# Kernel tuning notes

Measured on AMD Instinct MI355X. Metric: run time of the kernel, lower is better.

## Reference

```python
import jax, jax.numpy as jnp
import numpy as np

E, D_IN, D_OUT, RANK, ALPHA = 8, 2048, 2048, 8, 8.0
SCALING = ALPHA / RANK


def setup_inputs() -> dict:
    key = jax.random.key(0)
    ks = jax.random.split(key, 7)
    x = jax.random.normal(ks[0], (2, 4096, D_IN), dtype=jnp.float32)
    # base linear fc: weight [d_out, d_in], bias [d_out]
    Wf = jax.random.normal(ks[1], (D_OUT, D_IN), dtype=jnp.float32) / np.sqrt(D_IN)
    bf = jax.random.normal(ks[2], (D_OUT,), dtype=jnp.float32) * 0.01
    # router: weight [E, d_in], bias [E]
    Wr = jax.random.normal(ks[3], (E, D_IN), dtype=jnp.float32) / np.sqrt(D_IN)
    br = jnp.zeros((E,), dtype=jnp.float32)
    # stacked LoRA factors: A [E, rank, d_in] (kaiming-uniform-like), B [E, d_out, rank]
    # (original inits lora_B to zeros; use small random values so grads are non-trivial)
    A = jax.random.uniform(ks[4], (E, RANK, D_IN), dtype=jnp.float32,
                           minval=-1.0, maxval=1.0) / np.sqrt(D_IN)
    Bm = jax.random.normal(ks[5], (E, D_OUT, RANK), dtype=jnp.float32) * 0.02
    return {"x": x, "Wf": Wf, "bf": bf, "Wr": Wr, "br": br, "A": A, "Bm": Bm}


def reference(x, Wf, bf, Wr, br, A, Bm):
    # base output: x @ Wf^T + bf  -> [B, T, d_out]
    base = jnp.einsum('btd,od->bto', x, Wf) + bf
    # router softmax over experts -> [B, T, E]
    logits = jnp.einsum('btd,ed->bte', x, Wr) + br
    w = jax.nn.softmax(logits, axis=-1)
    # all-expert low-rank projection: h = x @ A_e^T -> [B, T, E, rank]
    h = jnp.einsum('btd,erd->bter', x, A)
    # up-project and fuse routing-weighted accumulation -> [B, T, d_out]
    lora = SCALING * jnp.einsum('bter,eor,bte->bto', h, Bm, w)
    return base + lora, w
```

## Files before the change

### kernel.cpp

```cpp
#include <hip/hip_runtime.h>
#include <hip/hip_bf16.h>

#define BT      8192
#define DIN     2048
#define DOUT    2048
#define NEXP    8
#define RANK    8
#define KX      2112
#define NSPLIT  4
#define HLD     72
#define SCALING 1.0f
#define SLOT    32768

typedef __bf16 bf16x8 __attribute__((ext_vector_type(8)));
typedef __bf16 bf16x4 __attribute__((ext_vector_type(4)));
typedef float  f32x4  __attribute__((ext_vector_type(4)));

#define XB_OFF     0
#define XB_BYTES   (BT * KX * 2)
#define WB_OFF     (XB_OFF + XB_BYTES)
#define WB_BYTES   (DOUT * KX * 2)
#define ACAT_OFF   (WB_OFF + WB_BYTES)
#define ACAT_BYTES (128 * DIN * 2)
#define HP_OFF     (ACAT_OFF + ACAT_BYTES)
#define HP_BYTES   (NSPLIT * BT * HLD * 4)

__device__ __forceinline__ void gload_lds16(const void* g, void* l) {
    __builtin_amdgcn_global_load_lds(
        (__attribute__((address_space(1))) void*)(g),
        (__attribute__((address_space(3))) void*)(l),
        16, 0, 0);
}

#define MFMA16(a, b, c) __builtin_amdgcn_mfma_f32_16x16x32_bf16((a), (b), (c), 0, 0, 0)

__global__ __launch_bounds__(256) void mole_prep(
    const float* __restrict__ Wf, const float* __restrict__ Bm,
    const float* __restrict__ Wr, const float* __restrict__ A,
    __bf16* __restrict__ WB, __bf16* __restrict__ ACAT)
{
    const int i = blockIdx.x * 256 + threadIdx.x;
    const int R1 = DOUT * (DIN / 4);
    const int R2 = DOUT * 64;
    if (i < R1) {
        const int o = i >> 9, c4 = i & 511;
        float4 v = ((const float4*)Wf)[(size_t)o * 512 + c4];
        bf16x4 b; b[0] = (__bf16)v.x; b[1] = (__bf16)v.y; b[2] = (__bf16)v.z; b[3] = (__bf16)v.w;
        *(bf16x4*)&WB[(size_t)o * KX + (c4 << 2)] = b;
    } else if (i < R1 + R2) {
        const int j = i - R1;
        const int o = j >> 6, c = j & 63;
        const int e = c >> 3, r = c & 7;
        WB[(size_t)o * KX + DIN + c] = (__bf16)Bm[((size_t)e * DOUT + o) * RANK + r];
    } else {
        const int j = i - (R1 + R2);
        const int r = j >> 9, c4 = j & 511;
        float4 v;
        if (r < 8)        v = ((const float4*)Wr)[(size_t)r * 512 + c4];
        else if (r < 72)  v = ((const float4*)A)[(size_t)(r - 8) * 512 + c4];
        else              v = make_float4(0.f, 0.f, 0.f, 0.f);
        bf16x4 b; b[0] = (__bf16)v.x; b[1] = (__bf16)v.y; b[2] = (__bf16)v.z; b[3] = (__bf16)v.w;
        *(bf16x4*)&ACAT[(size_t)r * DIN + (c4 << 2)] = b;
    }
}

__global__ __launch_bounds__(256) void mole_hconv(
    const float* __restrict__ x, const __bf16* __restrict__ ACAT,
    __bf16* __restrict__ XB, float* __restrict__ HP)
{
    __shared__ __align__(16) __bf16 Xs[128][32];
    __shared__ __align__(16) __bf16 Bs[128][32];

    const int tid = threadIdx.x;
    const int wv  = tid >> 6, ln = tid & 63;
    const int wr  = wv >> 1, wc = wv & 1;
    const size_t m0 = (size_t)blockIdx.x * 128;
    const int kStart = blockIdx.z * (DIN / NSPLIT);
    float* C = HP + (size_t)blockIdx.z * BT * HLD;

    const int xr = tid >> 3;
    const int xc = (tid & 7) << 2;
    const float* gx  = x  + (m0 + xr) * (size_t)DIN + kStart + xc;
    __bf16*      gxb = XB + (m0 + xr) * (size_t)KX  + kStart + xc;

    const int srow = (wv << 4) + (ln >> 2);
    const int scol = (ln & 3) << 3;
    const __bf16* gB0 = ACAT + srow * (size_t)DIN + kStart + scol;
    const __bf16* gB1 = gB0 + (size_t)64 * DIN;
    __bf16* lB0 = &Bs[(wv << 4)][0];
    __bf16* lB1 = &Bs[64 + (wv << 4)][0];

    f32x4 acc[4][4] = {};
    const int fr = ln & 15;
    const int fk = (ln >> 4) << 3;

    for (int ks = 0; ks < (DIN / NSPLIT) / 32; ++ks) {
        gload_lds16(gB0, lB0);
        gload_lds16(gB1, lB1);
        gB0 += 32; gB1 += 32;
        #pragma unroll
        for (int j = 0; j < 4; ++j) {
            float4 v = *(const float4*)(gx + (size_t)(32 * j) * DIN + 32 * ks);
            bf16x4 b; b[0] = (__bf16)v.x; b[1] = (__bf16)v.y;
            b[2] = (__bf16)v.z; b[3] = (__bf16)v.w;
            *(bf16x4*)&Xs[xr + 32 * j][xc] = b;
            *(bf16x4*)(gxb + (size_t)(32 * j) * KX + 32 * ks) = b;
        }
        __syncthreads();

        bf16x8 af[4], bfr[4];
        #pragma unroll
        for (int m = 0; m < 4; ++m)
            af[m] = *(const bf16x8*)&Xs[(wr << 6) + (m << 4) + fr][fk];
        #pragma unroll
        for (int n = 0; n < 4; ++n)
            bfr[n] = *(const bf16x8*)&Bs[(wc << 6) + (n << 4) + fr][fk];
        #pragma unroll
        for (int m = 0; m < 4; ++m)
            #pragma unroll
            for (int n = 0; n < 4; ++n)
                acc[m][n] = MFMA16(af[m], bfr[n], acc[m][n]);
        __syncthreads();
    }

    const int cr = (ln >> 4) << 2;
    const int cc = ln & 15;
    #pragma unroll
    for (int n = 0; n < 4; ++n) {
        const int col = (wc << 6) + (n << 4) + cc;
        if (col < HLD) {
            #pragma unroll
            for (int m = 0; m < 4; ++m) {
                const size_t row = m0 + (wr << 6) + (m << 4) + cr;
                #pragma unroll
                for (int r = 0; r < 4; ++r)
                    C[(row + r) * (size_t)HLD + col] = acc[m][n][r];
            }
        }
    }
}

__global__ __launch_bounds__(256) void mole_softmax_g(
    const float* __restrict__ HP, const float* __restrict__ br,
    float* __restrict__ wOut, __bf16* __restrict__ XB)
{
    const int t   = blockIdx.x * 4 + (threadIdx.x >> 6);
    const int tid = threadIdx.x & 63;
    float h = 0.0f;
    #pragma unroll
    for (int sp = 0; sp < NSPLIT; ++sp)
        h += HP[((size_t)sp * BT + t) * HLD + 8 + tid];

    float lg[NEXP];
    #pragma unroll
    for (int e = 0; e < NEXP; ++e) {
        lg[e] = br[e];
        #pragma unroll
        for (int sp = 0; sp < NSPLIT; ++sp)
            lg[e] += HP[((size_t)sp * BT + t) * HLD + e];
    }
    float mx = lg[0];
    #pragma unroll
    for (int e = 1; e < NEXP; ++e) mx = fmaxf(mx, lg[e]);
    float ex[NEXP], den = 0.0f;
    #pragma unroll
    for (int e = 0; e < NEXP; ++e) { ex[e] = expf(lg[e] - mx); den += ex[e]; }

    const float w_my = ex[tid >> 3] / den;
    XB[(size_t)t * KX + DIN + tid] = (__bf16)(SCALING * w_my * h);
    if (tid < NEXP) wOut[(size_t)t * NEXP + tid] = ex[tid] / den;
}

__global__ __launch_bounds__(512, 1) void mole_gemm256(
    const __bf16* __restrict__ XBp, const __bf16* __restrict__ WBp,
    float* __restrict__ C, const float* __restrict__ bias)
{
    __shared__ __align__(16) char smem[131072];

    const int tid = threadIdx.x;
    const int wv  = tid >> 6, l = tid & 63;
    const int wm  = wv >> 2, wn = wv & 3;
    const int bid = blockIdx.x;
    const int xcd = bid & 7, ib = bid >> 3;
    const int tm = xcd * 4 + (ib & 3), tn = ib >> 2;
    const size_t m0 = (size_t)tm * 256, n0 = (size_t)tn * 256;

    const int op = wv >> 2, ww = wv & 3;
    const __bf16* gstage = (op == 0 ? XBp + (m0 + ww * 64) * KX
                                    : WBp + (n0 + ww * 64) * KX)
                         + (size_t)(l >> 2) * KX + (((l & 3) ^ ((l >> 3) & 3)) << 3);
    const int stageBase = op * 16384 + ww * 4096;

    const int fr = l & 15, fq = l >> 4;
    const int swz = (fq ^ ((fr >> 1) & 3)) << 4;
    const int aByte = (wm * 128 + fr) * 64 + swz;
    const int bByte = 16384 + (wn * 64 + fr) * 64 + swz;

    f32x4 acc[8][4] = {};
    bf16x8 fa0[8], fb0[4], fa1[8], fb1[4];

#define STAGE(S)                                                              \
    {                                                                         \
        char* dst = smem + ((S) & 3) * SLOT + stageBase;                      \
        const __bf16* g = gstage + (size_t)(S) * 32;                          \
        _Pragma("unroll")                                                     \
        for (int j = 0; j < 4; ++j)                                           \
            gload_lds16(g + (size_t)j * 16 * KX, dst + j * 1024);             \
    }

#define READS(S, FA, FB)                                                      \
    {                                                                         \
        const char* slot = smem + ((S) & 3) * SLOT;                           \
        _Pragma("unroll")                                                     \
        for (int nf = 0; nf < 4; ++nf)                                        \
            FB[nf] = *(const bf16x8*)(slot + bByte + nf * 1024);              \
        _Pragma("unroll")                                                     \
        for (int mf = 0; mf < 8; ++mf)                                        \
            FA[mf] = *(const bf16x8*)(slot + aByte + mf * 1024);              \
    }

#define STEP(S, VMN, DOSTAGE, DOREAD, FAc, FBc, FAn, FBn)                     \
    {                                                                         \
        asm volatile("s_waitcnt vmcnt(" #VMN ")" ::: "memory");               \
        __builtin_amdgcn_s_barrier();                                         \
        if (DOREAD) READS((S) + 1, FAn, FBn);                                 \
        if (DOSTAGE) STAGE((S) + 3);                                          \
        __builtin_amdgcn_sched_barrier(0);                                    \
        __builtin_amdgcn_s_setprio(1);                                        \
        _Pragma("unroll")                                                     \
        for (int mf = 0; mf < 8; ++mf)                                        \
            _Pragma("unroll")                                                 \
            for (int nf = 0; nf < 4; ++nf)                                    \
                acc[mf][nf] = MFMA16(FAc[mf], FBc[nf], acc[mf][nf]);          \
        __builtin_amdgcn_s_setprio(0);                                        \
    }

    STAGE(0); STAGE(1); STAGE(2);
    asm volatile("s_waitcnt vmcnt(8)" ::: "memory");
    __builtin_amdgcn_s_barrier();
    READS(0, fa0, fb0);

    #pragma unroll 1
    for (int s = 0; s < 62; s += 2) {
        STEP(s,     4, true, true, fa0, fb0, fa1, fb1);
        STEP(s + 1, 4, true, true, fa1, fb1, fa0, fb0);
    }
    STEP(62, 4, true,  true,  fa0, fb0, fa1, fb1);
    STEP(63, 4, false, true,  fa1, fb1, fa0, fb0);
    STEP(64, 0, false, true,  fa0, fb0, fa1, fb1);
    STEP(65, 0, false, false, fa1, fb1, fa0, fb0);
#undef STEP
#undef READS
#undef STAGE

    const size_t crow = m0 + wm * 128 + fq * 4;
    const size_t ccol = n0 + wn * 64 + fr;
    #pragma unroll
    for (int nf = 0; nf < 4; ++nf) {
        const float bv = bias[ccol + nf * 16];
        #pragma unroll
        for (int mf = 0; mf < 8; ++mf) {
            float* cp = C + (crow + (size_t)mf * 16) * DOUT + ccol + nf * 16;
            #pragma unroll
            for (int i = 0; i < 4; ++i)
                cp[(size_t)i * DOUT] = acc[mf][nf][i] + bv;
        }
    }
}

extern "C" void kernel_launch(void* const* d_in, const int* in_sizes, int n_in,
                              void* d_out, int out_size, void* d_ws, size_t ws_size,
                              hipStream_t stream) {
    const float* x  = (const float*)d_in[0];
    const float* Wf = (const float*)d_in[1];
    const float* bf = (const float*)d_in[2];
    const float* Wr = (const float*)d_in[3];
    const float* br = (const float*)d_in[4];
    const float* A  = (const float*)d_in[5];
    const float* Bm = (const float*)d_in[6];

    float* out0 = (float*)d_out;
    float* wOut = out0 + (size_t)BT * DOUT;

    char* ws = (char*)d_ws;
    __bf16* XB   = (__bf16*)(ws + XB_OFF);
    __bf16* WB   = (__bf16*)(ws + WB_OFF);
    __bf16* ACAT = (__bf16*)(ws + ACAT_OFF);
    float*  HP   = (float*)(ws + HP_OFF);

    mole_prep<<<4864, 256, 0, stream>>>(Wf, Bm, Wr, A, WB, ACAT);
    mole_hconv<<<dim3(64, 1, NSPLIT), 256, 0, stream>>>(x, ACAT, XB, HP);
    mole_softmax_g<<<BT / 4, 256, 0, stream>>>(HP, br, wOut, XB);
    mole_gemm256<<<256, 512, 0, stream>>>(XB, WB, out0, bf);
}
```

Before: 103.5 us.

## Restructure GEMM main loop into K=64 double-buffered quarter-tile ping-pong schedule

Replaces the 4-slot K=32 LDS ring with two 64 KB buffers holding K=64 tiles, using a new XOR swizzle over 128-byte rows. Each K-tile's MFMA work is split into four quadrant phases interleaved with partial global-to-LDS loads for the next tile and barrier/waitcnt fences. The aim is to halve the number of iterations, cut per-K-step barrier overhead, and better overlap loads with MFMA. The cost is more barriers per tile and a hand-tuned waitcnt schedule that is fragile to get right.

```diff
diff --git a/kernel.cpp b/kernel.cpp
--- a/kernel.cpp
+++ b/kernel.cpp
@@ -10,7 +10,6 @@
 #define NSPLIT  4
 #define HLD     72
 #define SCALING 1.0f
-#define SLOT    32768
 
 typedef __bf16 bf16x8 __attribute__((ext_vector_type(8)));
 typedef __bf16 bf16x4 __attribute__((ext_vector_type(4)));
@@ -185,73 +184,136 @@
     const int tm = xcd * 4 + (ib & 3), tn = ib >> 2;
     const size_t m0 = (size_t)tm * 256, n0 = (size_t)tn * 256;
 
-    const int op = wv >> 2, ww = wv & 3;
-    const __bf16* gstage = (op == 0 ? XBp + (m0 + ww * 64) * KX
-                                    : WBp + (n0 + ww * 64) * KX)
-                         + (size_t)(l >> 2) * KX + (((l & 3) ^ ((l >> 3) & 3)) << 3);
-    const int stageBase = op * 16384 + ww * 4096;
+    const __bf16* gA = XBp + (m0 + (l >> 3)) * KX + (((l & 7) ^ (l >> 3)) << 3);
+    const __bf16* gB = WBp + (n0 + (l >> 3)) * KX + (((l & 7) ^ (l >> 3)) << 3);
+    const int wv8 = wv * 8;
+    const int rbB = ((wv & 3) * 8) + ((wv >> 2) * 64);
 
     const int fr = l & 15, fq = l >> 4;
-    const int swz = (fq ^ ((fr >> 1) & 3)) << 4;
-    const int aByte = (wm * 128 + fr) * 64 + swz;
-    const int bByte = 16384 + (wn * 64 + fr) * 64 + swz;
+    const int sw0 = ((fq)     ^ (fr & 7)) << 4;
+    const int sw1 = ((4 + fq) ^ (fr & 7)) << 4;
+    const int aOff = (wm * 128 + fr) * 128;
+    const int bOff = 32768 + (wn * 64 + fr) * 128;
 
     f32x4 acc[8][4] = {};
-    bf16x8 fa0[8], fb0[4], fa1[8], fb1[4];
-
-#define STAGE(S)                                                              \
-    {                                                                         \
-        char* dst = smem + ((S) & 3) * SLOT + stageBase;                      \
-        const __bf16* g = gstage + (size_t)(S) * 32;                          \
+    bf16x8 fa[4][2], fa2[4][2], fb[2][2], fb2[2][2];
+
+#define GLA(RB, T, BUF)                                                       \
+    gload_lds16(gA + (size_t)((RB) + wv8) * KX + (size_t)(T) * 64,            \
+                smem + (BUF) * 65536 + ((RB) + wv8) * 128)
+#define GLB(RB, T, BUF)                                                       \
+    gload_lds16(gB + (size_t)((RB) + rbB) * KX + (size_t)(T) * 64,            \
+                smem + (BUF) * 65536 + 32768 + ((RB) + rbB) * 128)
+#define ST_AQ1(T, BUF) { GLA(0, T, BUF);  GLA(128, T, BUF); }
+#define ST_AQ2(T, BUF) { GLA(64, T, BUF); GLA(192, T, BUF); }
+#define ST_BH1(T, BUF) { GLB(0, T, BUF);  GLB(128, T, BUF); }
+#define ST_BH2(T, BUF) { GLB(32, T, BUF); GLB(160, T, BUF); }
+
+#define RD_FA(ARR, B0, PB)                                                    \
+    _Pragma("unroll")                                                         \
+    for (int mf = 0; mf < 4; ++mf) {                                          \
+        const char* a_ = smem + (PB) * 65536 + aOff + ((B0) + mf) * 2048;     \
+        ARR[mf][0] = *(const bf16x8*)(a_ + sw0);                              \
+        ARR[mf][1] = *(const bf16x8*)(a_ + sw1);                              \
+    }
+#define RD_FB(ARR, B0, PB)                                                    \
+    _Pragma("unroll")                                                         \
+    for (int nf = 0; nf < 2; ++nf) {                                          \
+        const char* b_ = smem + (PB) * 65536 + bOff + ((B0) + nf) * 2048;     \
+        ARR[nf][0] = *(const bf16x8*)(b_ + sw0);                              \
+        ARR[nf][1] = *(const bf16x8*)(b_ + sw1);                              \
+    }
+#define MM(FA, FB, MB, NB)                                                    \
+    __builtin_amdgcn_s_setprio(1);                                            \
+    _Pragma("unroll")                                                         \
+    for (int kk = 0; kk < 2; ++kk)                                            \
         _Pragma("unroll")                                                     \
-        for (int j = 0; j < 4; ++j)                                           \
-            gload_lds16(g + (size_t)j * 16 * KX, dst + j * 1024);             \
-    }
-
-#define READS(S, FA, FB)                                                      \
-    {                                                                         \
-        const char* slot = smem + ((S) & 3) * SLOT;                           \
-        _Pragma("unroll")                                                     \
-        for (int nf = 0; nf < 4; ++nf)                                        \
-            FB[nf] = *(const bf16x8*)(slot + bByte + nf * 1024);              \
-        _Pragma("unroll")                                                     \
-        for (int mf = 0; mf < 8; ++mf)                                        \
-            FA[mf] = *(const bf16x8*)(slot + aByte + mf * 1024);              \
-    }
-
-#define STEP(S, VMN, DOSTAGE, DOREAD, FAc, FBc, FAn, FBn)                     \
-    {                                                                         \
-        asm volatile("s_waitcnt vmcnt(" #VMN ")" ::: "memory");               \
-        __builtin_amdgcn_s_barrier();                                         \
-        if (DOREAD) READS((S) + 1, FAn, FBn);                                 \
-        if (DOSTAGE) STAGE((S) + 3);                                          \
-        __builtin_amdgcn_sched_barrier(0);                                    \
-        __builtin_amdgcn_s_setprio(1);                                        \
-        _Pragma("unroll")                                                     \
-        for (int mf = 0; mf < 8; ++mf)                                        \
+        for (int mf = 0; mf < 4; ++mf)                                        \
             _Pragma("unroll")                                                 \
-            for (int nf = 0; nf < 4; ++nf)                                    \
-                acc[mf][nf] = MFMA16(FAc[mf], FBc[nf], acc[mf][nf]);          \
-        __builtin_amdgcn_s_setprio(0);                                        \
-    }
-
-    STAGE(0); STAGE(1); STAGE(2);
-    asm volatile("s_waitcnt vmcnt(8)" ::: "memory");
-    __builtin_amdgcn_s_barrier();
-    READS(0, fa0, fb0);
+            for (int nf = 0; nf < 2; ++nf)                                    \
+                acc[(MB) + mf][(NB) + nf] =                                   \
+                    MFMA16(FA[mf][kk], FB[nf][kk], acc[(MB) + mf][(NB) + nf]);\
+    __builtin_amdgcn_s_setprio(0);
+#define MIDBAR { __builtin_amdgcn_s_barrier();                                \
+                 asm volatile("s_waitcnt lgkmcnt(0)" ::: "memory");           \
+                 __builtin_amdgcn_sched_barrier(0); }
+#define ENDBAR __builtin_amdgcn_s_barrier();
+#define LG8    asm volatile("s_waitcnt lgkmcnt(8)" ::: "memory");
+#define VMC(N) asm volatile("s_waitcnt vmcnt(" #N ")" ::: "memory");
+
+    ST_AQ1(0, 0); ST_BH1(0, 0); ST_BH2(0, 0); ST_AQ2(0, 0);
+    ST_AQ1(1, 1); ST_BH1(1, 1); ST_BH2(1, 1);
+    VMC(6); ENDBAR;
 
     #pragma unroll 1
-    for (int s = 0; s < 62; s += 2) {
-        STEP(s,     4, true, true, fa0, fb0, fa1, fb1);
-        STEP(s + 1, 4, true, true, fa1, fb1, fa0, fb0);
-    }
-    STEP(62, 4, true,  true,  fa0, fb0, fa1, fb1);
-    STEP(63, 4, false, true,  fa1, fb1, fa0, fb0);
-    STEP(64, 0, false, true,  fa0, fb0, fa1, fb1);
-    STEP(65, 0, false, false, fa1, fb1, fa0, fb0);
-#undef STEP
-#undef READS
-#undef STAGE
+    for (int i = 0; i < 15; ++i) {
+        const int t = 2 * i;
+        RD_FA(fa, 0, 0); RD_FB(fb, 0, 0);
+        ST_AQ2(t + 1, 1);
+        LG8; MIDBAR; MM(fa, fb, 0, 0); ENDBAR;
+        RD_FB(fb2, 2, 0);
+        ST_AQ1(t + 2, 0);
+        MIDBAR; MM(fa, fb2, 0, 2); ENDBAR;
+        RD_FA(fa2, 4, 0);
+        ST_BH1(t + 2, 0);
+        MIDBAR; MM(fa2, fb, 4, 0); ENDBAR;
+        ST_BH2(t + 2, 0);
+        MIDBAR; MM(fa2, fb2, 4, 2); VMC(6); ENDBAR;
+        RD_FA(fa, 0, 1); RD_FB(fb, 0, 1);
+        ST_AQ2(t + 2, 0);
+        LG8; MIDBAR; MM(fa, fb, 0, 0); ENDBAR;
+        RD_FB(fb2, 2, 1);
+        ST_AQ1(t + 3, 1);
+        MIDBAR; MM(fa, fb2, 0, 2); ENDBAR;
+        RD_FA(fa2, 4, 1);
+        ST_BH1(t + 3, 1);
+        MIDBAR; MM(fa2, fb, 4, 0); ENDBAR;
+        ST_BH2(t + 3, 1);
+        MIDBAR; MM(fa2, fb2, 4, 2); VMC(6); ENDBAR;
+    }
+    {
+        RD_FA(fa, 0, 0); RD_FB(fb, 0, 0);
+        ST_AQ2(31, 1);
+        LG8; MIDBAR; MM(fa, fb, 0, 0); ENDBAR;
+        RD_FB(fb2, 2, 0);
+        ST_AQ1(32, 0);
+        MIDBAR; MM(fa, fb2, 0, 2); ENDBAR;
+        RD_FA(fa2, 4, 0);
+        ST_BH1(32, 0);
+        MIDBAR; MM(fa2, fb, 4, 0); ENDBAR;
+        ST_BH2(32, 0);
+        MIDBAR; MM(fa2, fb2, 4, 2); VMC(6); ENDBAR;
+        RD_FA(fa, 0, 1); RD_FB(fb, 0, 1);
+        ST_AQ2(32, 0);
+        LG8; MIDBAR; MM(fa, fb, 0, 0); ENDBAR;
+        RD_FB(fb2, 2, 1);
+        MIDBAR; MM(fa, fb2, 0, 2); ENDBAR;
+        RD_FA(fa2, 4, 1);
+        MIDBAR; MM(fa2, fb, 4, 0); ENDBAR;
+        MIDBAR; MM(fa2, fb2, 4, 2); VMC(4); ENDBAR;
+    }
+    {
+        RD_FA(fa, 0, 0); RD_FB(fb, 0, 0);
+        LG8; MIDBAR; MM(fa, fb, 0, 0); VMC(2); ENDBAR;
+        RD_FB(fb2, 2, 0);
+        MIDBAR; MM(fa, fb2, 0, 2); VMC(0); ENDBAR;
+        RD_FA(fa2, 4, 0);
+        MIDBAR; MM(fa2, fb, 4, 0); ENDBAR;
+        MM(fa2, fb2, 4, 2);
+    }
+#undef GLA
+#undef GLB
+#undef ST_AQ1
+#undef ST_AQ2
+#undef ST_BH1
+#undef ST_BH2
+#undef RD_FA
+#undef RD_FB
+#undef MM
+#undef MIDBAR
+#undef ENDBAR
+#undef LG8
+#undef VMC
 
     const size_t crow = m0 + wm * 128 + fq * 4;
     const size_t ccol = n0 + wn * 64 + fr;
```

After: 100.9 us (median of 3 runs). 1.03x faster.

## Fuse router/LoRA-A projection with softmax and gating into one kernel

Applied to the files above, without the earlier changes.

Replaces the split-K hconv kernel and the separate softmax kernel with one kernel that processes 16 tokens per block over the full K range. Router softmax and the gated LoRA intermediate are computed in shared memory and written straight into the bf16 activation buffer. This drops the fp32 partial-sum workspace round-trip and one launch, and gives 512 blocks instead of 256. The cost is that every block re-reads the whole 128x2048 ACAT matrix and issues only two MFMAs per K step per wave, so the kernel may be bound by loads and barriers.

```diff
diff --git a/kernel.cpp b/kernel.cpp
--- a/kernel.cpp
+++ b/kernel.cpp
@@ -7,8 +7,6 @@
 #define NEXP    8
 #define RANK    8
 #define KX      2112
-#define NSPLIT  4
-#define HLD     72
 #define SCALING 1.0f
 #define SLOT    32768
 
@@ -22,8 +20,6 @@
 #define WB_BYTES   (DOUT * KX * 2)
 #define ACAT_OFF   (WB_OFF + WB_BYTES)
 #define ACAT_BYTES (128 * DIN * 2)
-#define HP_OFF     (ACAT_OFF + ACAT_BYTES)
-#define HP_BYTES   (NSPLIT * BT * HLD * 4)
 
 __device__ __forceinline__ void gload_lds16(const void* g, void* l) {
     __builtin_amdgcn_global_load_lds(
@@ -64,111 +60,103 @@
     }
 }
 
-__global__ __launch_bounds__(256) void mole_hconv(
+__global__ __launch_bounds__(256) void mole_hfuse(
     const float* __restrict__ x, const __bf16* __restrict__ ACAT,
-    __bf16* __restrict__ XB, float* __restrict__ HP)
+    const float* __restrict__ br,
+    __bf16* __restrict__ XB, float* __restrict__ wOut)
 {
-    __shared__ __align__(16) __bf16 Xs[128][32];
     __shared__ __align__(16) __bf16 Bs[128][32];
+    __shared__ __align__(16) __bf16 Xs[16][32];
+    __shared__ float hbuf[16][80];
+    __shared__ float wl[16][8];
 
     const int tid = threadIdx.x;
     const int wv  = tid >> 6, ln = tid & 63;
-    const int wr  = wv >> 1, wc = wv & 1;
-    const size_t m0 = (size_t)blockIdx.x * 128;
-    const int kStart = blockIdx.z * (DIN / NSPLIT);
-    float* C = HP + (size_t)blockIdx.z * BT * HLD;
-
-    const int xr = tid >> 3;
-    const int xc = (tid & 7) << 2;
-    const float* gx  = x  + (m0 + xr) * (size_t)DIN + kStart + xc;
-    __bf16*      gxb = XB + (m0 + xr) * (size_t)KX  + kStart + xc;
+    const size_t t0 = (size_t)blockIdx.x * 16;
 
     const int srow = (wv << 4) + (ln >> 2);
     const int scol = (ln & 3) << 3;
-    const __bf16* gB0 = ACAT + srow * (size_t)DIN + kStart + scol;
+    const __bf16* gB0 = ACAT + srow * (size_t)DIN + scol;
     const __bf16* gB1 = gB0 + (size_t)64 * DIN;
     __bf16* lB0 = &Bs[(wv << 4)][0];
     __bf16* lB1 = &Bs[64 + (wv << 4)][0];
 
-    f32x4 acc[4][4] = {};
+    const int xr = tid >> 3;
+    const int xc = (tid & 7) << 2;
+    const float* gx  = x  + (t0 + xr) * (size_t)DIN + xc;
+    __bf16*      gxb = XB + (t0 + xr) * (size_t)KX  + xc;
+
     const int fr = ln & 15;
     const int fk = (ln >> 4) << 3;
 
-    for (int ks = 0; ks < (DIN / NSPLIT) / 32; ++ks) {
-        gload_lds16(gB0, lB0);
-        gload_lds16(gB1, lB1);
-        gB0 += 32; gB1 += 32;
+    f32x4 acc0 = {}, acc1 = {};
+
+    for (int ks = 0; ks < DIN / 32; ++ks) {
+        const int kb = ks * 32;
+        gload_lds16(gB0 + kb, lB0);
+        gload_lds16(gB1 + kb, lB1);
+        if (tid < 128) {
+            float4 v = *(const float4*)(gx + kb);
+            bf16x4 b; b[0] = (__bf16)v.x; b[1] = (__bf16)v.y;
+            b[2] = (__bf16)v.z; b[3] = (__bf16)v.w;
+            *(bf16x4*)&Xs[xr][xc] = b;
+            *(bf16x4*)(gxb + kb) = b;
+        }
+        __syncthreads();
+
+        bf16x8 fa = *(const bf16x8*)&Xs[fr][fk];
+        bf16x8 fb0 = *(const bf16x8*)&Bs[(wv << 5) + fr][fk];
+        bf16x8 fb1 = *(const bf16x8*)&Bs[(wv << 5) + 16 + fr][fk];
+        acc0 = MFMA16(fa, fb0, acc0);
+        acc1 = MFMA16(fa, fb1, acc1);
+        __syncthreads();
+    }
+
+    const int crow = (ln >> 4) << 2;
+    const int ccol = ln & 15;
+    {
+        const int c0 = (wv << 5) + ccol;
+        if (c0 < 72) {
+            #pragma unroll
+            for (int r = 0; r < 4; ++r) hbuf[crow + r][c0] = acc0[r];
+        }
+        const int c1 = (wv << 5) + 16 + ccol;
+        if (c1 < 72) {
+            #pragma unroll
+            for (int r = 0; r < 4; ++r) hbuf[crow + r][c1] = acc1[r];
+        }
+    }
+    __syncthreads();
+
+    if (tid < 128) {
+        const int tok = tid >> 3, e = tid & 7;
+        float lg = hbuf[tok][e] + br[e];
+        float mx = lg;
+        mx = fmaxf(mx, __shfl_xor(mx, 1));
+        mx = fmaxf(mx, __shfl_xor(mx, 2));
+        mx = fmaxf(mx, __shfl_xor(mx, 4));
+        float ex = expf(lg - mx);
+        float sm = ex;
+        sm += __shfl_xor(sm, 1);
+        sm += __shfl_xor(sm, 2);
+        sm += __shfl_xor(sm, 4);
+        const float w = ex / sm;
+        wl[tok][e] = w;
+        wOut[(t0 + tok) * NEXP + e] = w;
+    }
+    __syncthreads();
+
+    {
+        const int tok = tid >> 4;
+        const int c0  = (tid & 15) << 2;
+        bf16x4 g4;
         #pragma unroll
         for (int j = 0; j < 4; ++j) {
-            float4 v = *(const float4*)(gx + (size_t)(32 * j) * DIN + 32 * ks);
-            bf16x4 b; b[0] = (__bf16)v.x; b[1] = (__bf16)v.y;
-            b[2] = (__bf16)v.z; b[3] = (__bf16)v.w;
-            *(bf16x4*)&Xs[xr + 32 * j][xc] = b;
-            *(bf16x4*)(gxb + (size_t)(32 * j) * KX + 32 * ks) = b;
-        }
-        __syncthreads();
-
-        bf16x8 af[4], bfr[4];
-        #pragma unroll
-        for (int m = 0; m < 4; ++m)
-            af[m] = *(const bf16x8*)&Xs[(wr << 6) + (m << 4) + fr][fk];
-        #pragma unroll
-        for (int n = 0; n < 4; ++n)
-            bfr[n] = *(const bf16x8*)&Bs[(wc << 6) + (n << 4) + fr][fk];
-        #pragma unroll
-        for (int m = 0; m < 4; ++m)
-            #pragma unroll
-            for (int n = 0; n < 4; ++n)
-                acc[m][n] = MFMA16(af[m], bfr[n], acc[m][n]);
-        __syncthreads();
-    }
-
-    const int cr = (ln >> 4) << 2;
-    const int cc = ln & 15;
-    #pragma unroll
-    for (int n = 0; n < 4; ++n) {
-        const int col = (wc << 6) + (n << 4) + cc;
-        if (col < HLD) {
-            #pragma unroll
-            for (int m = 0; m < 4; ++m) {
-                const size_t row = m0 + (wr << 6) + (m << 4) + cr;
-                #pragma unroll
-                for (int r = 0; r < 4; ++r)
-                    C[(row + r) * (size_t)HLD + col] = acc[m][n][r];
-            }
-        }
-    }
-}
-
-__global__ __launch_bounds__(256) void mole_softmax_g(
-    const float* __restrict__ HP, const float* __restrict__ br,
-    float* __restrict__ wOut, __bf16* __restrict__ XB)
-{
-    const int t   = blockIdx.x * 4 + (threadIdx.x >> 6);
-    const int tid = threadIdx.x & 63;
-    float h = 0.0f;
-    #pragma unroll
-    for (int sp = 0; sp < NSPLIT; ++sp)
-        h += HP[((size_t)sp * BT + t) * HLD + 8 + tid];
-
-    float lg[NEXP];
-    #pragma unroll
-    for (int e = 0; e < NEXP; ++e) {
-        lg[e] = br[e];
-        #pragma unroll
-        for (int sp = 0; sp < NSPLIT; ++sp)
-            lg[e] += HP[((size_t)sp * BT + t) * HLD + e];
-    }
-    float mx = lg[0];
-    #pragma unroll
-    for (int e = 1; e < NEXP; ++e) mx = fmaxf(mx, lg[e]);
-    float ex[NEXP], den = 0.0f;
-    #pragma unroll
-    for (int e = 0; e < NEXP; ++e) { ex[e] = expf(lg[e] - mx); den += ex[e]; }
-
-    const float w_my = ex[tid >> 3] / den;
-    XB[(size_t)t * KX + DIN + tid] = (__bf16)(SCALING * w_my * h);
-    if (tid < NEXP) wOut[(size_t)t * NEXP + tid] = ex[tid] / den;
+            const int c = c0 + j;
+            g4[j] = (__bf16)(SCALING * wl[tok][c >> 3] * hbuf[tok][8 + c]);
+        }
+        *(bf16x4*)&XB[(t0 + tok) * KX + DIN + c0] = g4;
+    }
 }
 
 __global__ __launch_bounds__(512, 1) void mole_gemm256(
@@ -286,10 +274,8 @@
     __bf16* XB   = (__bf16*)(ws + XB_OFF);
     __bf16* WB   = (__bf16*)(ws + WB_OFF);
     __bf16* ACAT = (__bf16*)(ws + ACAT_OFF);
-    float*  HP   = (float*)(ws + HP_OFF);
 
     mole_prep<<<4864, 256, 0, stream>>>(Wf, Bm, Wr, A, WB, ACAT);
-    mole_hconv<<<dim3(64, 1, NSPLIT), 256, 0, stream>>>(x, ACAT, XB, HP);
-    mole_softmax_g<<<BT / 4, 256, 0, stream>>>(HP, br, wOut, XB);
+    mole_hfuse<<<BT / 16, 256, 0, stream>>>(x, ACAT, br, XB, wOut);
     mole_gemm256<<<256, 512, 0, stream>>>(XB, WB, out0, bf);
 }
```

Result: slower. 119.5 us (+15.5%).

## Shrink GEMM tile to 128x256 with 3-slot LDS ring for multi-block occupancy

Applied to the files above, without the earlier changes.

Replaces the 256x256 single-block-per-CU GEMM with a 128x256 tile, 512 blocks, a 3-stage LDS ring of 24 KB slots (72 KB total), and launch bounds allowing several blocks per CU. The register double-buffered fragment prefetch is dropped in favour of loading fragments after each barrier, relying on co-resident blocks to hide latency. This raises the wave count available to overlap loads and MFMAs. In exchange it halves arithmetic intensity per tile, so the shared W operand is re-read more often and more global traffic is issued.

```diff
diff --git a/kernel.cpp b/kernel.cpp
--- a/kernel.cpp
+++ b/kernel.cpp
@@ -7,10 +7,12 @@
 #define NEXP    8
 #define RANK    8
 #define KX      2112
+#define NSUB    66
 #define NSPLIT  4
 #define HLD     72
 #define SCALING 1.0f
-#define SLOT    32768
+#define SLOTSZ  24576
+#define LDSZ    73728
 
 typedef __bf16 bf16x8 __attribute__((ext_vector_type(8)));
 typedef __bf16 bf16x4 __attribute__((ext_vector_type(4)));
@@ -171,95 +173,101 @@
     if (tid < NEXP) wOut[(size_t)t * NEXP + tid] = ex[tid] / den;
 }
 
-__global__ __launch_bounds__(512, 1) void mole_gemm256(
+__global__ __launch_bounds__(512, 4) void mole_gemm128x256(
     const __bf16* __restrict__ XBp, const __bf16* __restrict__ WBp,
     float* __restrict__ C, const float* __restrict__ bias)
 {
-    __shared__ __align__(16) char smem[131072];
+    __shared__ __align__(16) char smem[LDSZ];
 
     const int tid = threadIdx.x;
     const int wv  = tid >> 6, l = tid & 63;
     const int wm  = wv >> 2, wn = wv & 3;
     const int bid = blockIdx.x;
     const int xcd = bid & 7, ib = bid >> 3;
-    const int tm = xcd * 4 + (ib & 3), tn = ib >> 2;
-    const size_t m0 = (size_t)tm * 256, n0 = (size_t)tn * 256;
-
-    const int op = wv >> 2, ww = wv & 3;
-    const __bf16* gstage = (op == 0 ? XBp + (m0 + ww * 64) * KX
-                                    : WBp + (n0 + ww * 64) * KX)
-                         + (size_t)(l >> 2) * KX + (((l & 3) ^ ((l >> 3) & 3)) << 3);
-    const int stageBase = op * 16384 + ww * 4096;
+    const int tm = xcd * 8 + (ib & 7), tn = ib >> 3;
+    const size_t m0 = (size_t)tm * 128, n0 = (size_t)tn * 256;
+
+    const int swcol = ((l & 3) ^ ((l >> 3) & 3)) << 3;
+    const __bf16* gsA  = XBp + (m0 + 16 * wv + (l >> 2)) * (size_t)KX + swcol;
+    const __bf16* gsB0 = WBp + (n0 + 32 * wv + (l >> 2)) * (size_t)KX + swcol;
+    const __bf16* gsB1 = gsB0 + (size_t)16 * KX;
+    const int dA  = wv * 1024;
+    const int dB0 = 8192 + wv * 2048;
+    const int dB1 = dB0 + 1024;
 
     const int fr = l & 15, fq = l >> 4;
     const int swz = (fq ^ ((fr >> 1) & 3)) << 4;
-    const int aByte = (wm * 128 + fr) * 64 + swz;
-    const int bByte = 16384 + (wn * 64 + fr) * 64 + swz;
-
-    f32x4 acc[8][4] = {};
-    bf16x8 fa0[8], fb0[4], fa1[8], fb1[4];
-
-#define STAGE(S)                                                              \
+    const int aBase = (wm * 64 + fr) * 64 + swz;
+    const int bBase = 8192 + (wn * 64 + fr) * 64 + swz;
+
+    f32x4 acc[4][4] = {};
+
+#define STAGE(STB)                                                            \
     {                                                                         \
-        char* dst = smem + ((S) & 3) * SLOT + stageBase;                      \
-        const __bf16* g = gstage + (size_t)(S) * 32;                          \
-        _Pragma("unroll")                                                     \
-        for (int j = 0; j < 4; ++j)                                           \
-            gload_lds16(g + (size_t)j * 16 * KX, dst + j * 1024);             \
-    }
-
-#define READS(S, FA, FB)                                                      \
-    {                                                                         \
-        const char* slot = smem + ((S) & 3) * SLOT;                           \
-        _Pragma("unroll")                                                     \
-        for (int nf = 0; nf < 4; ++nf)                                        \
-            FB[nf] = *(const bf16x8*)(slot + bByte + nf * 1024);              \
-        _Pragma("unroll")                                                     \
-        for (int mf = 0; mf < 8; ++mf)                                        \
-            FA[mf] = *(const bf16x8*)(slot + aByte + mf * 1024);              \
-    }
-
-#define STEP(S, VMN, DOSTAGE, DOREAD, FAc, FBc, FAn, FBn)                     \
-    {                                                                         \
-        asm volatile("s_waitcnt vmcnt(" #VMN ")" ::: "memory");               \
-        __builtin_amdgcn_s_barrier();                                         \
-        if (DOREAD) READS((S) + 1, FAn, FBn);                                 \
-        if (DOSTAGE) STAGE((S) + 3);                                          \
-        __builtin_amdgcn_sched_barrier(0);                                    \
-        __builtin_amdgcn_s_setprio(1);                                        \
-        _Pragma("unroll")                                                     \
-        for (int mf = 0; mf < 8; ++mf)                                        \
-            _Pragma("unroll")                                                 \
-            for (int nf = 0; nf < 4; ++nf)                                    \
-                acc[mf][nf] = MFMA16(FAc[mf], FBc[nf], acc[mf][nf]);          \
-        __builtin_amdgcn_s_setprio(0);                                        \
-    }
-
-    STAGE(0); STAGE(1); STAGE(2);
-    asm volatile("s_waitcnt vmcnt(8)" ::: "memory");
-    __builtin_amdgcn_s_barrier();
-    READS(0, fa0, fb0);
-
+        gload_lds16(gsA,  smem + (STB) + dA);                                 \
+        gload_lds16(gsB0, smem + (STB) + dB0);                                \
+        gload_lds16(gsB1, smem + (STB) + dB1);                                \
+        gsA += 32; gsB0 += 32; gsB1 += 32;                                    \
+    }
+
+    STAGE(0); STAGE(SLOTSZ);
+
+    int sb = 0, st = 2 * SLOTSZ;
     #pragma unroll 1
-    for (int s = 0; s < 62; s += 2) {
-        STEP(s,     4, true, true, fa0, fb0, fa1, fb1);
-        STEP(s + 1, 4, true, true, fa1, fb1, fa0, fb0);
-    }
-    STEP(62, 4, true,  true,  fa0, fb0, fa1, fb1);
-    STEP(63, 4, false, true,  fa1, fb1, fa0, fb0);
-    STEP(64, 0, false, true,  fa0, fb0, fa1, fb1);
-    STEP(65, 0, false, false, fa1, fb1, fa0, fb0);
-#undef STEP
-#undef READS
+    for (int s = 0; s < NSUB - 2; ++s) {
+        asm volatile("s_waitcnt vmcnt(3)" ::: "memory");
+        __builtin_amdgcn_s_barrier();
+        bf16x8 fa[4], fb[4];
+        #pragma unroll
+        for (int nf = 0; nf < 4; ++nf)
+            fb[nf] = *(const bf16x8*)(smem + sb + bBase + nf * 1024);
+        #pragma unroll
+        for (int mf = 0; mf < 4; ++mf)
+            fa[mf] = *(const bf16x8*)(smem + sb + aBase + mf * 1024);
+        STAGE(st);
+        __builtin_amdgcn_sched_barrier(0);
+        __builtin_amdgcn_s_setprio(1);
+        #pragma unroll
+        for (int mf = 0; mf < 4; ++mf)
+            #pragma unroll
+            for (int nf = 0; nf < 4; ++nf)
+                acc[mf][nf] = MFMA16(fa[mf], fb[nf], acc[mf][nf]);
+        __builtin_amdgcn_s_setprio(0);
+        sb += SLOTSZ; if (sb >= LDSZ) sb = 0;
+        st += SLOTSZ; if (st >= LDSZ) st = 0;
+    }
+    #pragma unroll 1
+    for (int s = 0; s < 2; ++s) {
+        if (s == 0) asm volatile("s_waitcnt vmcnt(3)" ::: "memory");
+        else        asm volatile("s_waitcnt vmcnt(0)" ::: "memory");
+        __builtin_amdgcn_s_barrier();
+        bf16x8 fa[4], fb[4];
+        #pragma unroll
+        for (int nf = 0; nf < 4; ++nf)
+            fb[nf] = *(const bf16x8*)(smem + sb + bBase + nf * 1024);
+        #pragma unroll
+        for (int mf = 0; mf < 4; ++mf)
+            fa[mf] = *(const bf16x8*)(smem + sb + aBase + mf * 1024);
+        __builtin_amdgcn_s_setprio(1);
+        #pragma unroll
+        for (int mf = 0; mf < 4; ++mf)
+            #pragma unroll
+            for (int nf = 0; nf < 4; ++nf)
+                acc[mf][nf] = MFMA16(fa[mf], fb[nf], acc[mf][nf]);
+        __builtin_amdgcn_s_setprio(0);
+        sb += SLOTSZ; if (sb >= LDSZ) sb = 0;
+    }
 #undef STAGE
 
-    const size_t crow = m0 + wm * 128 + fq * 4;
-    const size_t ccol = n0 + wn * 64 + fr;
+    const int cr = (l >> 4) << 2;
+    const int cc = l & 15;
+    const size_t crow = m0 + wm * 64 + cr;
+    const size_t ccol = n0 + wn * 64 + cc;
     #pragma unroll
     for (int nf = 0; nf < 4; ++nf) {
         const float bv = bias[ccol + nf * 16];
         #pragma unroll
-        for (int mf = 0; mf < 8; ++mf) {
+        for (int mf = 0; mf < 4; ++mf) {
             float* cp = C + (crow + (size_t)mf * 16) * DOUT + ccol + nf * 16;
             #pragma unroll
             for (int i = 0; i < 4; ++i)
@@ -291,5 +299,5 @@
     mole_prep<<<4864, 256, 0, stream>>>(Wf, Bm, Wr, A, WB, ACAT);
     mole_hconv<<<dim3(64, 1, NSPLIT), 256, 0, stream>>>(x, ACAT, XB, HP);
     mole_softmax_g<<<BT / 4, 256, 0, stream>>>(HP, br, wOut, XB);
-    mole_gemm256<<<256, 512, 0, stream>>>(XB, WB, out0, bf);
-}
+    mole_gemm128x256<<<512, 512, 0, stream>>>(XB, WB, out0, bf);
+}
```

Result: slower. 111.9 us (+8.2%).
